# Kernel tuning notes

Hardware: AMD Instinct MI355X
Metric: run time of the kernel (lower is better)

Reference implementation:

```python
import jax, jax.numpy as jnp
import numpy as np

N_QUBITS = 16
N_LAYERS = 8
BATCH = 512


def _apply_1q(st, U, wire):
    """Apply a 2x2 (or batched [B,2,2]) unitary on `wire` of st [B]+[2]*n."""
    st2 = jnp.moveaxis(st, wire + 1, -1)
    if U.ndim == 3:  # batched (input-encoding) gate
        out = jnp.einsum('sab,s...b->s...a', U, st2)
    else:
        out = jnp.einsum('ab,...b->...a', U, st2)
    return jnp.moveaxis(out, -1, wire + 1)


def _apply_cnot(st, c, t):
    """CNOT(control=c, target=t) on st [B]+[2]*n; axis of wire w is w+1."""
    s0, s1 = jnp.split(st, 2, axis=c + 1)
    s1 = jnp.flip(s1, axis=t + 1)  # X on target within control=1 block
    return jnp.concatenate([s0, s1], axis=c + 1)


def _rot_mats(w):
    """PennyLane Rot(phi,theta,omega)=RZ(omega)RY(theta)RZ(phi); w:[n,3] -> [n,2,2]."""
    phi, theta, omega = w[:, 0], w[:, 1], w[:, 2]
    c = jnp.cos(theta / 2).astype(jnp.complex64)
    s = jnp.sin(theta / 2).astype(jnp.complex64)
    ep = jnp.exp(-0.5j * (phi + omega))  # complex64
    em = jnp.exp(-0.5j * (phi - omega))
    m00 = ep * c
    m01 = -jnp.conj(em) * s
    m10 = em * s
    m11 = jnp.conj(ep) * c
    return jnp.stack([jnp.stack([m00, m01], -1), jnp.stack([m10, m11], -1)], -2)


def _circuit(x, weights):
    B, n = x.shape
    # |0...0> state, shape [B] + [2]*n
    st = jnp.zeros((B,) + (2,) * n, jnp.complex64)
    st = st.at[(slice(None),) + (0,) * n].set(1.0)
    # RY(pi * x_i) encoding on each wire (batched gates)
    a = (jnp.pi * x) / 2
    ca, sa = jnp.cos(a), jnp.sin(a)
    for i in range(n):
        U = jnp.stack([jnp.stack([ca[:, i], -sa[:, i]], -1),
                       jnp.stack([sa[:, i], ca[:, i]], -1)], -2).astype(jnp.complex64)
        st = _apply_1q(st, U, i)
    # StronglyEntanglingLayers: per-layer Rot on each wire, then ring of CNOTs
    for l in range(N_LAYERS):
        mats = _rot_mats(weights[l])
        for i in range(n):
            st = _apply_1q(st, mats[i], i)
        r = (l % (n - 1)) + 1  # default PennyLane range pattern
        for i in range(n):
            st = _apply_cnot(st, i, (i + r) % n)
    # <Z_i> = P(bit_i = 0) - P(bit_i = 1)
    p = st.real ** 2 + st.imag ** 2
    outs = []
    for i in range(n):
        marg = jnp.sum(p, axis=tuple(ax for ax in range(1, n + 1) if ax != i + 1))  # [B,2]
        outs.append(marg[:, 0] - marg[:, 1])
    return jnp.stack(outs, axis=-1).astype(jnp.float32)  # [B, n]


def setup_inputs() -> dict:
    key = jax.random.key(0)
    k1, k2 = jax.random.split(key)
    x = jax.random.uniform(k1, (BATCH, N_QUBITS), dtype=jnp.float32)
    weights = jax.random.uniform(k2, (N_LAYERS, N_QUBITS, 3), dtype=jnp.float32)
    return {"x": x, "weights": weights}


def reference(x, weights):
    return _circuit(x, weights)
```

## Files before the change

### kernel.cpp

```cpp
#include <hip/hip_runtime.h>
#include <cstring>

#define NQ 16
#define NLAYERS 8
#define BATCHN 512
#define GROUPB 128
#define NGROUP (BATCHN/GROUPB)
#define LB 13
#define NLOC (1<<LB)
#define NCHUNK (1<<(NQ-LB))
#define NTHREADS 512

typedef unsigned u32;

struct PD {
  int layerA, layerB, mode, contig, b0;
  int qop[13];
  int glb[3];
  int r1dPos[2];
  int r1dQ[2];
  int r1lQ;
  int r1f[9];
  u32 tinv[13];
  u32 cinv[13];
};

__device__ __forceinline__ u32 swz(u32 q){ return q ^ ((q >> 3) & 7u); }

template<int J>
__device__ __forceinline__ void gate16(float2 (&a)[16],
  float M0r,float M0i,float M1r,float M1i,float M2r,float M2i,float M3r,float M3i){
  #pragma unroll
  for (int i=0;i<16;i++){
    if ((i>>J)&1) continue;
    const int i1 = i|(1<<J);
    float ar=a[i].x, ai=a[i].y, br=a[i1].x, bi=a[i1].y;
    a[i].x  = M0r*ar - M0i*ai + M1r*br - M1i*bi;
    a[i].y  = M0r*ai + M0i*ar + M1r*bi + M1i*br;
    a[i1].x = M2r*ar - M2i*ai + M3r*br - M3i*bi;
    a[i1].y = M2r*ai + M2i*ar + M3r*bi + M3i*br;
  }
}

__device__ __forceinline__ void lane_gate16(float2 (&a)[16], int tid, int j,
  float r0,float i0,float r1,float i1,float r2,float i2,float r3,float i3){
  int bit = (tid >> j) & 1;
  float cAr = bit? r3 : r0, cAi = bit? i3 : i0;
  float cBr = bit? r2 : r1, cBi = bit? i2 : i1;
  #pragma unroll
  for (int i=0;i<16;i++){
    float tx = __shfl_xor(a[i].x, 1<<j);
    float ty = __shfl_xor(a[i].y, 1<<j);
    float ax = a[i].x, ay = a[i].y;
    a[i].x = cAr*ax - cAi*ay + cBr*tx - cBi*ty;
    a[i].y = cAr*ay + cAi*ax + cBr*ty + cBi*tx;
  }
}

#define APPLY16(J, SRC) { \
  int _s = (SRC); \
  float r0_=__shfl(mm0,_s), i0_=__shfl(mm1,_s), r1_=__shfl(mm2,_s), i1_=__shfl(mm3,_s); \
  float r2_=__shfl(mm4,_s), i2_=__shfl(mm5,_s), r3_=__shfl(mm6,_s), i3_=__shfl(mm7,_s); \
  gate16<J>(a, r0_,i0_,r1_,i1_,r2_,i2_,r3_,i3_); }

#define LANE16(J, SRC) { \
  int _s = (SRC); \
  float r0_=__shfl(mm0,_s), i0_=__shfl(mm1,_s), r1_=__shfl(mm2,_s), i1_=__shfl(mm3,_s); \
  float r2_=__shfl(mm4,_s), i2_=__shfl(mm5,_s), r3_=__shfl(mm6,_s), i3_=__shfl(mm7,_s); \
  lane_gate16(a, tid, (J), r0_,i0_,r1_,i1_,r2_,i2_,r3_,i3_); }

__global__ __launch_bounds__(NTHREADS, 4)
void qpass(const float* __restrict__ x, const float* __restrict__ w,
           float2* __restrict__ state, float* __restrict__ out, PD pd)
{
  __shared__ __align__(16) float2 st[NLOC];
  const int tid = threadIdx.x;
  const u32 chunk = blockIdx.x;
  const int b = pd.b0 + blockIdx.y;
  float2* __restrict__ gst = state + ((size_t)b << NQ);

  float mm0,mm1,mm2,mm3,mm4,mm5,mm6,mm7;
  {
    int lane = tid & 63;
    int q = lane & 15;
    int lay = ((lane>>4)&1) ? pd.layerB : pd.layerA;
    if (lay < 0) lay = 0;
    float phi = w[(lay*NQ+q)*3+0], th = w[(lay*NQ+q)*3+1], om = w[(lay*NQ+q)*3+2];
    float sh, ch; sincosf(0.5f*th, &sh, &ch);
    float spo, cpo; sincosf(-0.5f*(phi+om), &spo, &cpo);
    float smo, cmo; sincosf(-0.5f*(phi-om), &smo, &cmo);
    mm0 =  cpo*ch; mm1 =  spo*ch;
    mm2 = -cmo*sh; mm3 =  smo*sh;
    mm4 =  cmo*sh; mm5 =  smo*sh;
    mm6 =  cpo*ch; mm7 = -spo*ch;
  }

  float2 a[16];

  if (pd.mode != 1){
    u32 ebase = 0, lbase = 0;
    #pragma unroll
    for (int j=0;j<9;j++) if ((tid>>j)&1){ ebase ^= 1u<<pd.qop[pd.r1f[j]]; lbase |= 1u<<pd.r1f[j]; }
    #pragma unroll
    for (int j=0;j<3;j++) if ((chunk>>j)&1) ebase ^= 1u<<pd.glb[j];
    u32 dm0 = 1u<<pd.qop[pd.r1dPos[0]], dm1 = 1u<<pd.qop[pd.r1dPos[1]];
    #pragma unroll
    for (int g=0; g<4; g++){
      u32 full = ebase ^ ((g&1)?dm0:0u) ^ (((g>>1)&1)?dm1:0u);
      const float4* gp = (const float4*)(gst + full);
      float4 v0 = gp[0], v1 = gp[1];
      a[g*4+0] = make_float2(v0.x,v0.y); a[g*4+1] = make_float2(v0.z,v0.w);
      a[g*4+2] = make_float2(v1.x,v1.y); a[g*4+3] = make_float2(v1.z,v1.w);
    }
    APPLY16(2, pd.r1dQ[0]);
    APPLY16(3, pd.r1dQ[1]);
    LANE16(0, pd.r1lQ);

    if (pd.mode == 2){
      float acc[NQ];
      #pragma unroll
      for (int q=0;q<NQ;q++) acc[q]=0.f;
      u32 nb = 0;
      #pragma unroll
      for (int j=0;j<9;j++) if ((tid>>j)&1) nb ^= pd.cinv[pd.r1f[j]];
      #pragma unroll
      for (int j=0;j<3;j++) if ((chunk>>j)&1) nb ^= 1u<<pd.glb[j];
      u32 cd0 = pd.cinv[pd.r1dPos[0]], cd1 = pd.cinv[pd.r1dPos[1]];
      #pragma unroll
      for (int g=0; g<4; g++){
        u32 n0 = nb ^ ((g&1)?cd0:0u) ^ (((g>>1)&1)?cd1:0u);
        #pragma unroll
        for (int e=0;e<4;e++){
          u32 n = n0 ^ ((e&1)?pd.cinv[0]:0u) ^ (((e>>1)&1)?pd.cinv[1]:0u);
          float2 v = a[g*4+e];
          float p = v.x*v.x + v.y*v.y;
          #pragma unroll
          for (int q=0;q<NQ;q++) acc[q] += ((n>>q)&1u) ? -p : p;
        }
      }
      #pragma unroll
      for (int q=0;q<NQ;q++){
        float v = acc[q];
        #pragma unroll
        for (int off=32; off; off>>=1) v += __shfl_xor(v, off);
        if ((tid & 63) == 0) atomicAdd(&out[b*NQ+q], v);
      }
      return;
    }

    u32 ld0 = 1u<<pd.r1dPos[0], ld1 = 1u<<pd.r1dPos[1];
    #pragma unroll
    for (int g=0; g<4; g++){
      u32 m = lbase | ((g&1)?ld0:0u) | (((g>>1)&1)?ld1:0u);
      u32 p2 = swz(m>>2)*2u;
      ((float4*)st)[p2  ] = make_float4(a[g*4+0].x,a[g*4+0].y,a[g*4+1].x,a[g*4+1].y);
      ((float4*)st)[p2+1] = make_float4(a[g*4+2].x,a[g*4+2].y,a[g*4+3].x,a[g*4+3].y);
    }
    __syncthreads();
  }

  u32 sb = 0;
  #pragma unroll
  for (int j=0;j<9;j++) if ((tid>>j)&1) sb ^= pd.tinv[2+j];
  u32 tD0 = pd.tinv[11], tD1 = pd.tinv[12];

  if (pd.mode == 1){
    float ca[NQ], sa[NQ];
    #pragma unroll
    for (int q=0;q<NQ;q++){
      float aa = 1.57079632679489662f * x[b*NQ+q];
      sincosf(aa, &sa[q], &ca[q]);
    }
    float vt = 1.f;
    #pragma unroll
    for (int j=0;j<9;j++){ int q = pd.qop[2+j]; vt *= ((tid>>j)&1)? sa[q] : ca[q]; }
    #pragma unroll
    for (int j=0;j<3;j++){ int q = pd.glb[j]; vt *= ((chunk>>j)&1)? sa[q] : ca[q]; }
    float c0 = ca[pd.qop[0]], s0 = sa[pd.qop[0]], c1 = ca[pd.qop[1]], s1 = sa[pd.qop[1]];
    float cd0 = ca[pd.qop[11]], sd0 = sa[pd.qop[11]];
    float cd1 = ca[pd.qop[12]], sd1 = sa[pd.qop[12]];
    #pragma unroll
    for (int g=0; g<4; g++){
      float vg = vt * ((g&1)? sd0 : cd0) * (((g>>1)&1)? sd1 : cd1);
      a[g*4+0] = make_float2(vg*c0*c1, 0.f);
      a[g*4+1] = make_float2(vg*s0*c1, 0.f);
      a[g*4+2] = make_float2(vg*c0*s1, 0.f);
      a[g*4+3] = make_float2(vg*s0*s1, 0.f);
    }
  } else {
    #pragma unroll
    for (int g=0; g<4; g++){
      u32 s = sb ^ ((g&1)?tD0:0u) ^ (((g>>1)&1)?tD1:0u);
      if (pd.contig){
        u32 p2 = swz(s>>2)*2u;
        float4 v0 = ((float4*)st)[p2], v1 = ((float4*)st)[p2+1];
        float2 w0=make_float2(v0.x,v0.y), w1=make_float2(v0.z,v0.w);
        float2 w2=make_float2(v1.x,v1.y), w3=make_float2(v1.z,v1.w);
        u32 sl = s & 3u;
        if (sl & 1){ float2 t=w0; w0=w1; w1=t; t=w2; w2=w3; w3=t; }
        if (sl & 2){ float2 t=w0; w0=w2; w2=t; t=w1; w1=w3; w3=t; }
        a[g*4+0]=w0; a[g*4+1]=w1; a[g*4+2]=w2; a[g*4+3]=w3;
      } else {
        #pragma unroll
        for (int e=0;e<4;e++){
          u32 se = s ^ ((e&1)?pd.tinv[0]:0u) ^ (((e>>1)&1)?pd.tinv[1]:0u);
          a[g*4+e] = st[swz(se>>2)*4u + (se&3u)];
        }
      }
    }
  }

  APPLY16(0, 16+pd.qop[0]);  APPLY16(1, 16+pd.qop[1]);
  APPLY16(2, 16+pd.qop[11]); APPLY16(3, 16+pd.qop[12]);
  #pragma unroll
  for (int j=0;j<6;j++){
    LANE16(j, 16+pd.qop[2+j]);
  }

  #pragma unroll
  for (int g=0; g<4; g++){
    u32 s = sb ^ ((g&1)?tD0:0u) ^ (((g>>1)&1)?tD1:0u);
    if (pd.contig){
      float2 w0=a[g*4+0], w1=a[g*4+1], w2=a[g*4+2], w3=a[g*4+3];
      u32 sl = s & 3u;
      if (sl & 1){ float2 t=w0; w0=w1; w1=t; t=w2; w2=w3; w3=t; }
      if (sl & 2){ float2 t=w0; w0=w2; w2=t; t=w1; w1=w3; w3=t; }
      u32 p2 = swz(s>>2)*2u;
      ((float4*)st)[p2  ] = make_float4(w0.x,w0.y,w1.x,w1.y);
      ((float4*)st)[p2+1] = make_float4(w2.x,w2.y,w3.x,w3.y);
    } else {
      #pragma unroll
      for (int e=0;e<4;e++){
        u32 se = s ^ ((e&1)?pd.tinv[0]:0u) ^ (((e>>1)&1)?pd.tinv[1]:0u);
        st[swz(se>>2)*4u + (se&3u)] = a[g*4+e];
      }
    }
  }
  __syncthreads();

  {
    u32 sb2 = 0;
    if (tid & 1) sb2 ^= pd.tinv[10];
    #pragma unroll
    for (int j=1;j<7;j++) if ((tid>>j)&1) sb2 ^= pd.tinv[1+j];
    if ((tid>>7)&1) sb2 ^= pd.tinv[11];
    if ((tid>>8)&1) sb2 ^= pd.tinv[12];
    u32 e0m = pd.tinv[8], e1m = pd.tinv[9];
    #pragma unroll
    for (int g=0; g<4; g++){
      u32 s = sb2 ^ ((g&1)?e0m:0u) ^ (((g>>1)&1)?e1m:0u);
      if (pd.contig){
        u32 p2 = swz(s>>2)*2u;
        float4 v0 = ((float4*)st)[p2], v1 = ((float4*)st)[p2+1];
        float2 w0=make_float2(v0.x,v0.y), w1=make_float2(v0.z,v0.w);
        float2 w2=make_float2(v1.x,v1.y), w3=make_float2(v1.z,v1.w);
        u32 sl = s & 3u;
        if (sl & 1){ float2 t=w0; w0=w1; w1=t; t=w2; w2=w3; w3=t; }
        if (sl & 2){ float2 t=w0; w0=w2; w2=t; t=w1; w1=w3; w3=t; }
        a[g*4+0]=w0; a[g*4+1]=w1; a[g*4+2]=w2; a[g*4+3]=w3;
      } else {
        #pragma unroll
        for (int e=0;e<4;e++){
          u32 se = s ^ ((e&1)?pd.tinv[0]:0u) ^ (((e>>1)&1)?pd.tinv[1]:0u);
          a[g*4+e] = st[swz(se>>2)*4u + (se&3u)];
        }
      }
    }
    APPLY16(2, 16+pd.qop[8]); APPLY16(3, 16+pd.qop[9]);
    LANE16(0, 16+pd.qop[10]);
    #pragma unroll
    for (int g=0; g<4; g++){
      u32 s = sb2 ^ ((g&1)?e0m:0u) ^ (((g>>1)&1)?e1m:0u);
      if (pd.contig){
        float2 w0=a[g*4+0], w1=a[g*4+1], w2=a[g*4+2], w3=a[g*4+3];
        u32 sl = s & 3u;
        if (sl & 1){ float2 t=w0; w0=w1; w1=t; t=w2; w2=w3; w3=t; }
        if (sl & 2){ float2 t=w0; w0=w2; w2=t; t=w1; w1=w3; w3=t; }
        u32 p2 = swz(s>>2)*2u;
        ((float4*)st)[p2  ] = make_float4(w0.x,w0.y,w1.x,w1.y);
        ((float4*)st)[p2+1] = make_float4(w2.x,w2.y,w3.x,w3.y);
      } else {
        #pragma unroll
        for (int e=0;e<4;e++){
          u32 se = s ^ ((e&1)?pd.tinv[0]:0u) ^ (((e>>1)&1)?pd.tinv[1]:0u);
          st[swz(se>>2)*4u + (se&3u)] = a[g*4+e];
        }
      }
    }
    __syncthreads();
  }

  {
    u32 ctid = 0, etid = 0;
    #pragma unroll
    for (int j=0;j<9;j++) if ((tid>>j)&1){ ctid ^= pd.cinv[2+j]; etid ^= 1u<<pd.qop[2+j]; }
    #pragma unroll
    for (int j=0;j<3;j++) if ((chunk>>j)&1) etid ^= 1u<<pd.glb[j];
    u32 c11 = pd.cinv[11], c12 = pd.cinv[12];
    u32 q11 = 1u<<pd.qop[11], q12 = 1u<<pd.qop[12];
    #pragma unroll
    for (int j=0;j<4;j++){
      u32 src   = ctid ^ ((j&1)?c11:0u) ^ (((j>>1)&1)?c12:0u);
      u32 ofull = etid ^ ((j&1)?q11:0u) ^ (((j>>1)&1)?q12:0u);
      u32 s0_ = src;
      u32 s1_ = src ^ pd.cinv[0];
      u32 s2_ = src ^ pd.cinv[1];
      u32 s3_ = src ^ pd.cinv[0] ^ pd.cinv[1];
      float2 vv0 = st[swz(s0_>>2)*4u + (s0_&3u)];
      float2 vv1 = st[swz(s1_>>2)*4u + (s1_&3u)];
      float2 vv2 = st[swz(s2_>>2)*4u + (s2_&3u)];
      float2 vv3 = st[swz(s3_>>2)*4u + (s3_&3u)];
      float4* gp = (float4*)(gst + ofull);
      gp[0] = make_float4(vv0.x,vv0.y,vv1.x,vv1.y);
      gp[1] = make_float4(vv2.x,vv2.y,vv3.x,vv3.y);
    }
  }
}

static const int Gs[9][3] = {
  {13,14,15},{9,10,11},{2,5,6},{4,7,13},{2,10,14},{6,8,11},{3,9,13},{5,7,14},{10,11,12}
};
static const int Dlen[8] = {4,9,10,10,9,10,9,6};
static const int Dl[8][10] = {
  {12,13,14,15,0,0,0,0,0,0},
  {7,8,9,10,11,12,13,14,15,0},
  {2,3,5,6,8,9,11,12,14,15},
  {0,3,4,7,8,9,11,12,13,15},
  {2,5,7,9,10,12,13,14,15,0},
  {0,2,5,6,8,10,11,12,14,15},
  {2,3,6,9,10,11,12,13,15,0},
  {5,6,7,13,14,15,0,0,0,0},
};

static inline u32 apply_cnot_idx(u32 v, int c, int t){ return v ^ (((v>>c)&1u)<<t); }

extern "C" void kernel_launch(void* const* d_in, const int* in_sizes, int n_in,
                              void* d_out, int out_size, void* d_ws, size_t ws_size,
                              hipStream_t stream)
{
  (void)in_sizes; (void)n_in; (void)ws_size;
  const float* x = (const float*)d_in[0];
  const float* w = (const float*)d_in[1];
  float* out = (float*)d_out;
  float2* state = (float2*)d_ws;

  hipMemsetAsync(d_out, 0, (size_t)out_size*sizeof(float), stream);

  for (int grp=0; grp<NGROUP; grp++){
    for (int p=0; p<9; p++){
      PD pd; memset(&pd, 0, sizeof(pd));
      pd.layerA = p-1;
      pd.layerB = (p<=7)? p : -1;
      pd.mode = (p==0)? 1 : ((p==8)? 2 : 0);
      pd.b0 = grp*GROUPB;

      u32 gm = 0;
      for (int i=0;i<3;i++){ pd.glb[i] = Gs[p][i]; gm |= 1u<<Gs[p][i]; }
      int np=0;
      for (int q=0;q<16;q++) if (!((gm>>q)&1u)) pd.qop[np++] = q;

      if (p >= 1){
        int pos[3], qq[3];
        for (int i=0;i<3;i++){
          int q = Gs[p-1][i]; qq[i] = q;
          int c=0; for (int k=0;k<q;k++) if ((gm>>k)&1u) c++;
          pos[i] = q - c;
        }
        for (int i=0;i<3;i++) for (int k=i+1;k<3;k++)
          if (pos[k] < pos[i]){ int t=pos[i];pos[i]=pos[k];pos[k]=t; t=qq[i];qq[i]=qq[k];qq[k]=t; }
        pd.r1lQ = qq[0];
        pd.r1dPos[0]=pos[1]; pd.r1dQ[0]=qq[1];
        pd.r1dPos[1]=pos[2]; pd.r1dQ[1]=qq[2];
        pd.r1f[0] = pos[0];
        int nf=1;
        for (int pp=2; pp<13; pp++)
          if (pp!=pos[0] && pp!=pos[1] && pp!=pos[2]) pd.r1f[nf++]=pp;
      } else {
        pd.r1lQ = 0;
        pd.r1dPos[0]=11; pd.r1dQ[0]=0;
        pd.r1dPos[1]=12; pd.r1dQ[1]=0;
        for (int j=0;j<9;j++) pd.r1f[j]=2+j;
      }

      if (p == 0){
        for (int bp=0;bp<13;bp++) pd.tinv[bp] = 1u<<bp;
      } else {
        int r = p;
        for (int bp=0;bp<13;bp++){
          u32 v = 1u<<pd.qop[bp];
          for (int i=Dlen[p-1]-1;i>=0;i--){ int c=Dl[p-1][i]; v = apply_cnot_idx(v, c, (c+r)&15); }
          u32 lv=0; for (int rr=0;rr<13;rr++) lv |= ((v>>pd.qop[rr])&1u)<<rr;
          pd.tinv[bp] = lv;
        }
      }
      pd.contig = (pd.tinv[0]==1u && pd.tinv[1]==2u) ? 1 : 0;

      if (p <= 7){
        int r = p+1;
        bool inD[16]; for (int i=0;i<16;i++) inD[i]=false;
        for (int i=0;i<Dlen[p];i++) inD[Dl[p][i]] = true;
        int A[16], na=0;
        for (int i=0;i<16;i++) if (!inD[i]) A[na++]=i;
        for (int bp=0;bp<13;bp++){
          u32 v = 1u<<pd.qop[bp];
          for (int i=na-1;i>=0;i--){ int c=A[i]; v = apply_cnot_idx(v, c, (c+r)&15); }
          if (p >= 1){
            int rp = p;
            for (int i=Dlen[p-1]-1;i>=0;i--){ int c=Dl[p-1][i]; v = apply_cnot_idx(v, c, (c+rp)&15); }
          }
          u32 lv=0; for (int rr=0;rr<13;rr++) lv |= ((v>>pd.qop[rr])&1u)<<rr;
          pd.cinv[bp] = lv;
        }
      } else {
        for (int bp=0;bp<13;bp++){
          u32 v = 1u<<pd.qop[bp];
          for (int i=0;i<Dlen[7];i++){ int c=Dl[7][i]; v = apply_cnot_idx(v, c, (c+8)&15); }
          pd.cinv[bp] = v;
        }
      }

      hipLaunchKernelGGL(qpass, dim3(NCHUNK, GROUPB), dim3(NTHREADS), 0, stream,
                         x, w, state, out, pd);
    }
  }
}
```

Baseline: 3.270 ms.

## Precompute swizzled LDS index masks on host and retune chunk qubit schedule

The host now folds the XOR swizzle into per-bit LDS address masks, because the swizzle is linear over XOR. The kernel can then compute shared-memory addresses with plain XORs, and the contig/non-contig branching and element swaps go away. The global-qubit groups and deferred-CNOT lists are re-planned so that chunk bits also feed into the local index, via the new tCkL and fCk masks. The lane position used for the first-stage gate changes as well. LDS accesses are now always scalar float2 rather than float4 when the layout is contiguous, which could change bank behaviour.

Result: faster. 2.911 ms (-11.0%).

```diff
diff --git a/kernel.cpp b/kernel.cpp
--- a/kernel.cpp
+++ b/kernel.cpp
@@ -14,7 +14,7 @@
 typedef unsigned u32;
 
 struct PD {
-  int layerA, layerB, mode, contig, b0;
+  int layerA, layerB, mode, b0;
   int qop[13];
   int glb[3];
   int r1dPos[2];
@@ -23,9 +23,15 @@
   int r1f[9];
   u32 tinv[13];
   u32 cinv[13];
+  u32 tL[13];
+  u32 cL[13];
+  u32 tCkL[3];
+  u32 fCk[3];
+  u32 r1em[9];
+  u32 r1eL[9];
+  u32 r1dm[2];
+  u32 r1dLm[2];
 };
-
-__device__ __forceinline__ u32 swz(u32 q){ return q ^ ((q >> 3) & 7u); }
 
 template<int J>
 __device__ __forceinline__ void gate16(float2 (&a)[16],
@@ -95,18 +101,22 @@
     mm6 =  cpo*ch; mm7 = -spo*ch;
   }
 
+  u32 ckL = 0;
+  if (chunk & 1) ckL ^= pd.tCkL[0];
+  if (chunk & 2) ckL ^= pd.tCkL[1];
+  if (chunk & 4) ckL ^= pd.tCkL[2];
+
   float2 a[16];
 
   if (pd.mode != 1){
-    u32 ebase = 0, lbase = 0;
-    #pragma unroll
-    for (int j=0;j<9;j++) if ((tid>>j)&1){ ebase ^= 1u<<pd.qop[pd.r1f[j]]; lbase |= 1u<<pd.r1f[j]; }
+    u32 ebase = 0, lbL = 0;
+    #pragma unroll
+    for (int j=0;j<9;j++) if ((tid>>j)&1){ ebase ^= pd.r1em[j]; lbL ^= pd.r1eL[j]; }
     #pragma unroll
     for (int j=0;j<3;j++) if ((chunk>>j)&1) ebase ^= 1u<<pd.glb[j];
-    u32 dm0 = 1u<<pd.qop[pd.r1dPos[0]], dm1 = 1u<<pd.qop[pd.r1dPos[1]];
-    #pragma unroll
-    for (int g=0; g<4; g++){
-      u32 full = ebase ^ ((g&1)?dm0:0u) ^ (((g>>1)&1)?dm1:0u);
+    #pragma unroll
+    for (int g=0; g<4; g++){
+      u32 full = ebase ^ ((g&1)?pd.r1dm[0]:0u) ^ (((g>>1)&1)?pd.r1dm[1]:0u);
       const float4* gp = (const float4*)(gst + full);
       float4 v0 = gp[0], v1 = gp[1];
       a[g*4+0] = make_float2(v0.x,v0.y); a[g*4+1] = make_float2(v0.z,v0.w);
@@ -114,7 +124,7 @@
     }
     APPLY16(2, pd.r1dQ[0]);
     APPLY16(3, pd.r1dQ[1]);
-    LANE16(0, pd.r1lQ);
+    LANE16(5, pd.r1lQ);
 
     if (pd.mode == 2){
       float acc[NQ];
@@ -124,7 +134,7 @@
       #pragma unroll
       for (int j=0;j<9;j++) if ((tid>>j)&1) nb ^= pd.cinv[pd.r1f[j]];
       #pragma unroll
-      for (int j=0;j<3;j++) if ((chunk>>j)&1) nb ^= 1u<<pd.glb[j];
+      for (int j=0;j<3;j++) if ((chunk>>j)&1) nb ^= pd.fCk[j];
       u32 cd0 = pd.cinv[pd.r1dPos[0]], cd1 = pd.cinv[pd.r1dPos[1]];
       #pragma unroll
       for (int g=0; g<4; g++){
@@ -148,21 +158,19 @@
       return;
     }
 
-    u32 ld0 = 1u<<pd.r1dPos[0], ld1 = 1u<<pd.r1dPos[1];
-    #pragma unroll
-    for (int g=0; g<4; g++){
-      u32 m = lbase | ((g&1)?ld0:0u) | (((g>>1)&1)?ld1:0u);
-      u32 p2 = swz(m>>2)*2u;
-      ((float4*)st)[p2  ] = make_float4(a[g*4+0].x,a[g*4+0].y,a[g*4+1].x,a[g*4+1].y);
-      ((float4*)st)[p2+1] = make_float4(a[g*4+2].x,a[g*4+2].y,a[g*4+3].x,a[g*4+3].y);
+    #pragma unroll
+    for (int g=0; g<4; g++){
+      u32 mL = lbL ^ ((g&1)?pd.r1dLm[0]:0u) ^ (((g>>1)&1)?pd.r1dLm[1]:0u);
+      ((float4*)st)[(mL>>1)  ] = make_float4(a[g*4+0].x,a[g*4+0].y,a[g*4+1].x,a[g*4+1].y);
+      ((float4*)st)[(mL>>1)+1] = make_float4(a[g*4+2].x,a[g*4+2].y,a[g*4+3].x,a[g*4+3].y);
     }
     __syncthreads();
   }
 
-  u32 sb = 0;
+  u32 sbL = ckL;
   #pragma unroll
-  for (int j=0;j<9;j++) if ((tid>>j)&1) sb ^= pd.tinv[2+j];
-  u32 tD0 = pd.tinv[11], tD1 = pd.tinv[12];
+  for (int j=0;j<9;j++) if ((tid>>j)&1) sbL ^= pd.tL[2+j];
+  const u32 Ltd0 = pd.tL[11], Ltd1 = pd.tL[12], Le0 = pd.tL[0], Le1 = pd.tL[1];
 
   if (pd.mode == 1){
     float ca[NQ], sa[NQ];
@@ -190,23 +198,11 @@
   } else {
     #pragma unroll
     for (int g=0; g<4; g++){
-      u32 s = sb ^ ((g&1)?tD0:0u) ^ (((g>>1)&1)?tD1:0u);
-      if (pd.contig){
-        u32 p2 = swz(s>>2)*2u;
-        float4 v0 = ((float4*)st)[p2], v1 = ((float4*)st)[p2+1];
-        float2 w0=make_float2(v0.x,v0.y), w1=make_float2(v0.z,v0.w);
-        float2 w2=make_float2(v1.x,v1.y), w3=make_float2(v1.z,v1.w);
-        u32 sl = s & 3u;
-        if (sl & 1){ float2 t=w0; w0=w1; w1=t; t=w2; w2=w3; w3=t; }
-        if (sl & 2){ float2 t=w0; w0=w2; w2=t; t=w1; w1=w3; w3=t; }
-        a[g*4+0]=w0; a[g*4+1]=w1; a[g*4+2]=w2; a[g*4+3]=w3;
-      } else {
-        #pragma unroll
-        for (int e=0;e<4;e++){
-          u32 se = s ^ ((e&1)?pd.tinv[0]:0u) ^ (((e>>1)&1)?pd.tinv[1]:0u);
-          a[g*4+e] = st[swz(se>>2)*4u + (se&3u)];
-        }
-      }
+      u32 sL = sbL ^ ((g&1)?Ltd0:0u) ^ (((g>>1)&1)?Ltd1:0u);
+      a[g*4+0] = st[sL];
+      a[g*4+1] = st[sL^Le0];
+      a[g*4+2] = st[sL^Le1];
+      a[g*4+3] = st[sL^Le0^Le1];
     }
   }
 
@@ -219,97 +215,60 @@
 
   #pragma unroll
   for (int g=0; g<4; g++){
-    u32 s = sb ^ ((g&1)?tD0:0u) ^ (((g>>1)&1)?tD1:0u);
-    if (pd.contig){
-      float2 w0=a[g*4+0], w1=a[g*4+1], w2=a[g*4+2], w3=a[g*4+3];
-      u32 sl = s & 3u;
-      if (sl & 1){ float2 t=w0; w0=w1; w1=t; t=w2; w2=w3; w3=t; }
-      if (sl & 2){ float2 t=w0; w0=w2; w2=t; t=w1; w1=w3; w3=t; }
-      u32 p2 = swz(s>>2)*2u;
-      ((float4*)st)[p2  ] = make_float4(w0.x,w0.y,w1.x,w1.y);
-      ((float4*)st)[p2+1] = make_float4(w2.x,w2.y,w3.x,w3.y);
-    } else {
-      #pragma unroll
-      for (int e=0;e<4;e++){
-        u32 se = s ^ ((e&1)?pd.tinv[0]:0u) ^ (((e>>1)&1)?pd.tinv[1]:0u);
-        st[swz(se>>2)*4u + (se&3u)] = a[g*4+e];
-      }
-    }
+    u32 sL = sbL ^ ((g&1)?Ltd0:0u) ^ (((g>>1)&1)?Ltd1:0u);
+    st[sL]         = a[g*4+0];
+    st[sL^Le0]     = a[g*4+1];
+    st[sL^Le1]     = a[g*4+2];
+    st[sL^Le0^Le1] = a[g*4+3];
   }
   __syncthreads();
 
   {
-    u32 sb2 = 0;
-    if (tid & 1) sb2 ^= pd.tinv[10];
-    #pragma unroll
-    for (int j=1;j<7;j++) if ((tid>>j)&1) sb2 ^= pd.tinv[1+j];
-    if ((tid>>7)&1) sb2 ^= pd.tinv[11];
-    if ((tid>>8)&1) sb2 ^= pd.tinv[12];
-    u32 e0m = pd.tinv[8], e1m = pd.tinv[9];
-    #pragma unroll
-    for (int g=0; g<4; g++){
-      u32 s = sb2 ^ ((g&1)?e0m:0u) ^ (((g>>1)&1)?e1m:0u);
-      if (pd.contig){
-        u32 p2 = swz(s>>2)*2u;
-        float4 v0 = ((float4*)st)[p2], v1 = ((float4*)st)[p2+1];
-        float2 w0=make_float2(v0.x,v0.y), w1=make_float2(v0.z,v0.w);
-        float2 w2=make_float2(v1.x,v1.y), w3=make_float2(v1.z,v1.w);
-        u32 sl = s & 3u;
-        if (sl & 1){ float2 t=w0; w0=w1; w1=t; t=w2; w2=w3; w3=t; }
-        if (sl & 2){ float2 t=w0; w0=w2; w2=t; t=w1; w1=w3; w3=t; }
-        a[g*4+0]=w0; a[g*4+1]=w1; a[g*4+2]=w2; a[g*4+3]=w3;
-      } else {
-        #pragma unroll
-        for (int e=0;e<4;e++){
-          u32 se = s ^ ((e&1)?pd.tinv[0]:0u) ^ (((e>>1)&1)?pd.tinv[1]:0u);
-          a[g*4+e] = st[swz(se>>2)*4u + (se&3u)];
-        }
-      }
+    u32 s2L = ckL;
+    if (tid & 1) s2L ^= pd.tL[10];
+    #pragma unroll
+    for (int j=1;j<7;j++) if ((tid>>j)&1) s2L ^= pd.tL[1+j];
+    if ((tid>>7)&1) s2L ^= pd.tL[11];
+    if ((tid>>8)&1) s2L ^= pd.tL[12];
+    const u32 LD0 = pd.tL[8], LD1 = pd.tL[9];
+    #pragma unroll
+    for (int g=0; g<4; g++){
+      u32 sL = s2L ^ ((g&1)?LD0:0u) ^ (((g>>1)&1)?LD1:0u);
+      a[g*4+0] = st[sL];
+      a[g*4+1] = st[sL^Le0];
+      a[g*4+2] = st[sL^Le1];
+      a[g*4+3] = st[sL^Le0^Le1];
     }
     APPLY16(2, 16+pd.qop[8]); APPLY16(3, 16+pd.qop[9]);
     LANE16(0, 16+pd.qop[10]);
     #pragma unroll
     for (int g=0; g<4; g++){
-      u32 s = sb2 ^ ((g&1)?e0m:0u) ^ (((g>>1)&1)?e1m:0u);
-      if (pd.contig){
-        float2 w0=a[g*4+0], w1=a[g*4+1], w2=a[g*4+2], w3=a[g*4+3];
-        u32 sl = s & 3u;
-        if (sl & 1){ float2 t=w0; w0=w1; w1=t; t=w2; w2=w3; w3=t; }
-        if (sl & 2){ float2 t=w0; w0=w2; w2=t; t=w1; w1=w3; w3=t; }
-        u32 p2 = swz(s>>2)*2u;
-        ((float4*)st)[p2  ] = make_float4(w0.x,w0.y,w1.x,w1.y);
-        ((float4*)st)[p2+1] = make_float4(w2.x,w2.y,w3.x,w3.y);
-      } else {
-        #pragma unroll
-        for (int e=0;e<4;e++){
-          u32 se = s ^ ((e&1)?pd.tinv[0]:0u) ^ (((e>>1)&1)?pd.tinv[1]:0u);
-          st[swz(se>>2)*4u + (se&3u)] = a[g*4+e];
-        }
-      }
+      u32 sL = s2L ^ ((g&1)?LD0:0u) ^ (((g>>1)&1)?LD1:0u);
+      st[sL]         = a[g*4+0];
+      st[sL^Le0]     = a[g*4+1];
+      st[sL^Le1]     = a[g*4+2];
+      st[sL^Le0^Le1] = a[g*4+3];
     }
     __syncthreads();
   }
 
   {
-    u32 ctid = 0, etid = 0;
-    #pragma unroll
-    for (int j=0;j<9;j++) if ((tid>>j)&1){ ctid ^= pd.cinv[2+j]; etid ^= 1u<<pd.qop[2+j]; }
+    u32 ctL = ckL, etid = 0;
+    #pragma unroll
+    for (int j=0;j<9;j++) if ((tid>>j)&1){ ctL ^= pd.cL[2+j]; etid ^= 1u<<pd.qop[2+j]; }
     #pragma unroll
     for (int j=0;j<3;j++) if ((chunk>>j)&1) etid ^= 1u<<pd.glb[j];
-    u32 c11 = pd.cinv[11], c12 = pd.cinv[12];
-    u32 q11 = 1u<<pd.qop[11], q12 = 1u<<pd.qop[12];
+    const u32 Lc0 = pd.cL[0], Lc1 = pd.cL[1];
+    const u32 Lc11 = pd.cL[11], Lc12 = pd.cL[12];
+    const u32 q11 = 1u<<pd.qop[11], q12 = 1u<<pd.qop[12];
     #pragma unroll
     for (int j=0;j<4;j++){
-      u32 src   = ctid ^ ((j&1)?c11:0u) ^ (((j>>1)&1)?c12:0u);
-      u32 ofull = etid ^ ((j&1)?q11:0u) ^ (((j>>1)&1)?q12:0u);
-      u32 s0_ = src;
-      u32 s1_ = src ^ pd.cinv[0];
-      u32 s2_ = src ^ pd.cinv[1];
-      u32 s3_ = src ^ pd.cinv[0] ^ pd.cinv[1];
-      float2 vv0 = st[swz(s0_>>2)*4u + (s0_&3u)];
-      float2 vv1 = st[swz(s1_>>2)*4u + (s1_&3u)];
-      float2 vv2 = st[swz(s2_>>2)*4u + (s2_&3u)];
-      float2 vv3 = st[swz(s3_>>2)*4u + (s3_&3u)];
+      u32 srcL  = ctL  ^ ((j&1)?Lc11:0u) ^ (((j>>1)&1)?Lc12:0u);
+      u32 ofull = etid ^ ((j&1)?q11:0u)  ^ (((j>>1)&1)?q12:0u);
+      float2 vv0 = st[srcL];
+      float2 vv1 = st[srcL^Lc0];
+      float2 vv2 = st[srcL^Lc1];
+      float2 vv3 = st[srcL^Lc0^Lc1];
       float4* gp = (float4*)(gst + ofull);
       gp[0] = make_float4(vv0.x,vv0.y,vv1.x,vv1.y);
       gp[1] = make_float4(vv2.x,vv2.y,vv3.x,vv3.y);
@@ -318,21 +277,23 @@
 }
 
 static const int Gs[9][3] = {
-  {13,14,15},{9,10,11},{2,5,6},{4,7,13},{2,10,14},{6,8,11},{3,9,13},{5,7,14},{10,11,12}
+  {13,14,15},{8,10,12},{11,13,15},{8,9,10},{7,11,15},{8,9,10},{11,12,13},{8,9,10},{13,14,15}
 };
-static const int Dlen[8] = {4,9,10,10,9,10,9,6};
+static const int Dlen[8] = {4,5,7,9,8,10,8,6};
 static const int Dl[8][10] = {
   {12,13,14,15,0,0,0,0,0,0},
-  {7,8,9,10,11,12,13,14,15,0},
-  {2,3,5,6,8,9,11,12,14,15},
-  {0,3,4,7,8,9,11,12,13,15},
-  {2,5,7,9,10,12,13,14,15,0},
-  {0,2,5,6,8,10,11,12,14,15},
-  {2,3,6,9,10,11,12,13,15,0},
-  {5,6,7,13,14,15,0,0,0,0},
+  {6,8,10,12,14,0,0,0,0,0},
+  {8,10,11,12,13,14,15,0,0,0},
+  {4,5,6,8,9,10,12,13,14,0},
+  {2,6,7,10,11,12,13,15,0,0},
+  {2,3,4,8,9,10,12,13,14,15},
+  {4,5,6,11,12,13,14,15,0,0},
+  {0,1,2,8,9,10,0,0,0,0},
 };
 
 static inline u32 apply_cnot_idx(u32 v, int c, int t){ return v ^ (((v>>c)&1u)<<t); }
+static inline u32 h_swz(u32 q){ return q ^ ((q>>3)&7u); }
+static inline u32 h_Lmap(u32 m){ return (h_swz(m>>2)<<2) | (m&3u); }
 
 extern "C" void kernel_launch(void* const* d_in, const int* in_sizes, int n_in,
                               void* d_out, int out_size, void* d_ws, size_t ws_size,
@@ -371,19 +332,23 @@
         pd.r1lQ = qq[0];
         pd.r1dPos[0]=pos[1]; pd.r1dQ[0]=qq[1];
         pd.r1dPos[1]=pos[2]; pd.r1dQ[1]=qq[2];
-        pd.r1f[0] = pos[0];
-        int nf=1;
+        int free_[9], nf=0;
         for (int pp=2; pp<13; pp++)
-          if (pp!=pos[0] && pp!=pos[1] && pp!=pos[2]) pd.r1f[nf++]=pp;
+          if (pp!=pos[0] && pp!=pos[1] && pp!=pos[2]) free_[nf++]=pp;
+        for (int j=0;j<5;j++) pd.r1f[j]=free_[j];
+        pd.r1f[5]=pos[0];
+        for (int j=0;j<3;j++) pd.r1f[6+j]=free_[5+j];
       } else {
         pd.r1lQ = 0;
         pd.r1dPos[0]=11; pd.r1dQ[0]=0;
         pd.r1dPos[1]=12; pd.r1dQ[1]=0;
-        for (int j=0;j<9;j++) pd.r1f[j]=2+j;
+        for (int j=0;j<5;j++) pd.r1f[j]=2+j;
+        pd.r1f[5]=10; pd.r1f[6]=7; pd.r1f[7]=8; pd.r1f[8]=9;
       }
 
       if (p == 0){
         for (int bp=0;bp<13;bp++) pd.tinv[bp] = 1u<<bp;
+        for (int j=0;j<3;j++) pd.tCkL[j] = 0u;
       } else {
         int r = p;
         for (int bp=0;bp<13;bp++){
@@ -392,8 +357,14 @@
           u32 lv=0; for (int rr=0;rr<13;rr++) lv |= ((v>>pd.qop[rr])&1u)<<rr;
           pd.tinv[bp] = lv;
         }
-      }
-      pd.contig = (pd.tinv[0]==1u && pd.tinv[1]==2u) ? 1 : 0;
+        for (int j=0;j<3;j++){
+          u32 v = 1u<<pd.glb[j];
+          for (int i=Dlen[p-1]-1;i>=0;i--){ int c=Dl[p-1][i]; v = apply_cnot_idx(v, c, (c+r)&15); }
+          v &= ~(1u<<pd.glb[j]);
+          u32 lv=0; for (int rr=0;rr<13;rr++) lv |= ((v>>pd.qop[rr])&1u)<<rr;
+          pd.tCkL[j] = h_Lmap(lv);
+        }
+      }
 
       if (p <= 7){
         int r = p+1;
@@ -411,12 +382,31 @@
           u32 lv=0; for (int rr=0;rr<13;rr++) lv |= ((v>>pd.qop[rr])&1u)<<rr;
           pd.cinv[bp] = lv;
         }
+        for (int j=0;j<3;j++) pd.fCk[j] = 0u;
       } else {
         for (int bp=0;bp<13;bp++){
           u32 v = 1u<<pd.qop[bp];
           for (int i=0;i<Dlen[7];i++){ int c=Dl[7][i]; v = apply_cnot_idx(v, c, (c+8)&15); }
           pd.cinv[bp] = v;
         }
+        for (int j=0;j<3;j++){
+          u32 v = 1u<<pd.glb[j];
+          for (int i=0;i<Dlen[7];i++){ int c=Dl[7][i]; v = apply_cnot_idx(v, c, (c+8)&15); }
+          pd.fCk[j] = v;
+        }
+      }
+
+      for (int k=0;k<13;k++){
+        pd.tL[k] = h_Lmap(pd.tinv[k]);
+        pd.cL[k] = (p<=7) ? h_Lmap(pd.cinv[k]) : 0u;
+      }
+      for (int j=0;j<9;j++){
+        pd.r1em[j] = 1u<<pd.qop[pd.r1f[j]];
+        pd.r1eL[j] = h_Lmap(1u<<pd.r1f[j]);
+      }
+      for (int j=0;j<2;j++){
+        pd.r1dm[j]  = 1u<<pd.qop[pd.r1dPos[j]];
+        pd.r1dLm[j] = h_Lmap(1u<<pd.r1dPos[j]);
       }
 
       hipLaunchKernelGGL(qpass, dim3(NCHUNK, GROUPB), dim3(NTHREADS), 0, stream,
```
